# Kernel optimization log

Measured on AMD Instinct MI355X. Metric: run time of the kernel, lower is better.

## Reference

```python
import jax, jax.numpy as jnp
import numpy as np

IGNORE_INDEX = -100


def setup_inputs() -> dict:
    key = jax.random.key(0)
    k1, k2, k3 = jax.random.split(key, 3)
    N, H, V = 4096, 1024, 32000
    x = jax.random.normal(k1, (N, H), dtype=jnp.float32)
    # lm_head weight, laid out [H, V] so logits = x @ weight (kernel's [D, V] layout)
    weight = jax.random.normal(k2, (H, V), dtype=jnp.float32) * (1.0 / np.sqrt(H))
    target = jax.random.randint(k3, (N,), 0, V)
    # exercise the ignore_index masking path
    target = target.at[:64].set(IGNORE_INDEX)
    return {"x": x, "weight": weight, "target": target}


def reference(x, weight, target):
    # Fused linear + cross entropy, reduction='sum'.
    # logits: [N, V] (the tensor the fused kernel tiles to avoid materializing)
    logits = jnp.dot(x, weight)
    lse = jax.nn.logsumexp(logits, axis=-1)                  # [N]
    valid = target != IGNORE_INDEX                            # [N]
    safe_labels = jnp.where(valid, target, 0)
    target_logits = jnp.take_along_axis(logits, safe_labels[:, None], axis=-1)[:, 0]
    vmask = valid.astype(logits.dtype)
    losses = (lse - target_logits) * vmask                    # [N], 0 where ignored
    lse_masked = lse * vmask
    # reduction == 'sum'
    return losses.sum(), lse_masked.sum()
```

## Files before the change

### kernel.cpp

```cpp
#include <hip/hip_runtime.h>
#include <hip/hip_bf16.h>

typedef float f32x4 __attribute__((ext_vector_type(4)));
typedef int i32x4v __attribute__((ext_vector_type(4)));
typedef int i32x8v __attribute__((ext_vector_type(8)));

#define IGNORE_INDEX (-100)
#define N_ROWS 4096
#define H_DIM  1024
#define V_DIM  32000

#define BM 128
#define BN 256
#define BK 128
#define NKT (H_DIM / BK)
#define CT_NUM (V_DIM / BN)
#define RT_NUM (N_ROWS / BM)
#define SCALE1 0x7f7f7f7f

#define XB8 (N_ROWS * H_DIM / (256 * 16))
__global__ __launch_bounds__(256) void k_prep(const float* __restrict__ x,
                                              const float* __restrict__ w,
                                              unsigned char* __restrict__ x8,
                                              unsigned char* __restrict__ wT8) {
  __shared__ float tile[128][65];
  const int t = threadIdx.x;
  if (blockIdx.x < XB8) {
    size_t i = ((size_t)blockIdx.x * 256 + t) * 16;
    const float4* xp = (const float4*)(x + i);
    float4 f0 = xp[0], f1 = xp[1], f2 = xp[2], f3 = xp[3];
    int4 o;
    int r;
    r = __builtin_amdgcn_cvt_pk_fp8_f32(f0.x, f0.y, 0, false);
    r = __builtin_amdgcn_cvt_pk_fp8_f32(f0.z, f0.w, r, true);
    o.x = r;
    r = __builtin_amdgcn_cvt_pk_fp8_f32(f1.x, f1.y, 0, false);
    r = __builtin_amdgcn_cvt_pk_fp8_f32(f1.z, f1.w, r, true);
    o.y = r;
    r = __builtin_amdgcn_cvt_pk_fp8_f32(f2.x, f2.y, 0, false);
    r = __builtin_amdgcn_cvt_pk_fp8_f32(f2.z, f2.w, r, true);
    o.z = r;
    r = __builtin_amdgcn_cvt_pk_fp8_f32(f3.x, f3.y, 0, false);
    r = __builtin_amdgcn_cvt_pk_fp8_f32(f3.z, f3.w, r, true);
    o.w = r;
    *(int4*)(x8 + i) = o;
    return;
  }
  const int b = blockIdx.x - XB8;
  const int v0 = (b % (V_DIM / 64)) * 64;
  const int k0 = (b / (V_DIM / 64)) * 128;
  {
    const int vq = t & 15;
    const int kr = t >> 4;
#pragma unroll
    for (int p = 0; p < 128; p += 16) {
      float4 v = *(const float4*)(w + (size_t)(k0 + kr + p) * V_DIM + v0 + vq * 4);
      tile[kr + p][vq * 4 + 0] = v.x;
      tile[kr + p][vq * 4 + 1] = v.y;
      tile[kr + p][vq * 4 + 2] = v.z;
      tile[kr + p][vq * 4 + 3] = v.w;
    }
  }
  __syncthreads();
  {
    const int vr = t >> 2;
    const int kq2 = t & 3;
#pragma unroll
    for (int h = 0; h < 2; ++h) {
      const int d4 = kq2 + h * 4;
      int4 o;
      int r;
#pragma unroll
      for (int d = 0; d < 4; ++d) {
        r = __builtin_amdgcn_cvt_pk_fp8_f32(tile[d4 * 16 + d * 4 + 0][vr],
                                            tile[d4 * 16 + d * 4 + 1][vr], 0, false);
        r = __builtin_amdgcn_cvt_pk_fp8_f32(tile[d4 * 16 + d * 4 + 2][vr],
                                            tile[d4 * 16 + d * 4 + 3][vr], r, true);
        ((int*)&o)[d] = r;
      }
      *(int4*)(wT8 + (size_t)(v0 + vr) * H_DIM + k0 + d4 * 16) = o;
    }
  }
}

__global__ __launch_bounds__(256) void k_gemm_lse(const unsigned char* __restrict__ A,
                                                  const unsigned char* __restrict__ Bt,
                                                  float* __restrict__ m_part,
                                                  float* __restrict__ s_part) {
  extern __shared__ __align__(16) unsigned char sMemRaw[];
#define SMA(buf) (sMemRaw + (buf) * 49152)
#define SMB(buf) (sMemRaw + (buf) * 49152 + 16384)
  float* maxbuf = (float*)sMemRaw;
  float* sumbuf = (float*)(sMemRaw + 2048);

  const int tid = threadIdx.x;
  const int wg = ((int)blockIdx.x & 7) * ((RT_NUM * CT_NUM) / 8) + ((int)blockIdx.x >> 3);
  const int rt = wg & (RT_NUM - 1);
  const int ct = wg >> 5;
  const int m0 = rt * BM;
  const int n0 = ct * BN;

  const int w = tid >> 6;
  const int l = tid & 63;
  const int wm = w >> 1;
  const int wn = w & 1;
  const int quad = l >> 4, lc = l & 15;

  f32x4 acc[4][8];
#pragma unroll
  for (int i = 0; i < 4; ++i)
#pragma unroll
    for (int j = 0; j < 8; ++j)
      acc[i][j] = (f32x4){0.f, 0.f, 0.f, 0.f};

  const int srow = tid >> 3;
  const int scol = ((tid & 7) ^ (srow & 7)) * 16;
  const unsigned char* ga = A + (size_t)(m0 + srow) * H_DIM + scol;
  const unsigned char* gb = Bt + (size_t)(n0 + srow) * H_DIM + scol;
  const int dOff = tid * 16;

  const int aoff = wm * 8192 + lc * 128;
  const int boff = wn * 16384 + lc * 128;
  const int sw0 = ((quad * 2) ^ (lc & 7)) * 16;
  const int sw1 = ((quad * 2 + 1) ^ (lc & 7)) * 16;

#define GLDS(gp, lp)                                                     \
  __builtin_amdgcn_global_load_lds(                                      \
      (const __attribute__((address_space(1))) void*)(gp),               \
      (__attribute__((address_space(3))) void*)(lp), 16, 0, 0)

#define STAGE12(buf, koff)                                               \
  do {                                                                   \
    _Pragma("unroll")                                                    \
    for (int i_ = 0; i_ < 4; ++i_)                                       \
      GLDS(ga + (size_t)i_ * 32 * H_DIM + (koff),                        \
           SMA(buf) + dOff + i_ * 4096);                                 \
    _Pragma("unroll")                                                    \
    for (int i_ = 0; i_ < 8; ++i_)                                       \
      GLDS(gb + (size_t)i_ * 32 * H_DIM + (koff),                        \
           SMB(buf) + dOff + i_ * 4096);                                 \
  } while (0)

#define LDA8(dst, buf, i)                                                \
  do {                                                                   \
    const unsigned char* p_ = SMA(buf) + (i) * 2048 + aoff;              \
    i32x4v lo_ = *(const i32x4v*)(p_ + sw0);                             \
    i32x4v hi_ = *(const i32x4v*)(p_ + sw1);                             \
    dst = __builtin_shufflevector(lo_, hi_, 0, 1, 2, 3, 4, 5, 6, 7);     \
  } while (0)

#define LDB8(dst, buf, j)                                                \
  do {                                                                   \
    const unsigned char* p_ = SMB(buf) + (j) * 2048 + boff;              \
    i32x4v lo_ = *(const i32x4v*)(p_ + sw0);                             \
    i32x4v hi_ = *(const i32x4v*)(p_ + sw1);                             \
    dst = __builtin_shufflevector(lo_, hi_, 0, 1, 2, 3, 4, 5, 6, 7);     \
  } while (0)

  STAGE12(0, 0);
  __syncthreads();

#pragma unroll
  for (int kt = 0; kt < NKT; ++kt) {
    const int cur = kt & 1;
    if (kt < NKT - 1) STAGE12(cur ^ 1, (kt + 1) * BK);

    i32x8v af[4];
    LDA8(af[0], cur, 0); LDA8(af[1], cur, 1);
    LDA8(af[2], cur, 2); LDA8(af[3], cur, 3);
#pragma unroll
    for (int j = 0; j < 8; ++j) {
      i32x8v bfj;
      LDB8(bfj, cur, j);
#pragma unroll
      for (int i = 0; i < 4; ++i)
        acc[i][j] = __builtin_amdgcn_mfma_scale_f32_16x16x128_f8f6f4(
            af[i], bfj, acc[i][j], 0, 0, 0, SCALE1, 0, SCALE1);
    }
    __syncthreads();
  }
#undef STAGE12
#undef GLDS
#undef LDA8
#undef LDB8

  float rmax[4][4];
#pragma unroll
  for (int i = 0; i < 4; ++i)
#pragma unroll
    for (int r = 0; r < 4; ++r) {
      float mx = acc[i][0][r];
#pragma unroll
      for (int j = 1; j < 8; ++j) mx = fmaxf(mx, acc[i][j][r]);
#pragma unroll
      for (int off = 1; off < 16; off <<= 1)
        mx = fmaxf(mx, __shfl_xor(mx, off, 64));
      rmax[i][r] = mx;
    }
  if (lc == 0) {
#pragma unroll
    for (int i = 0; i < 4; ++i)
#pragma unroll
      for (int r = 0; r < 4; ++r)
        maxbuf[(wm * 64 + i * 16 + quad * 4 + r) * 2 + wn] = rmax[i][r];
  }
  __syncthreads();
  float rowmax[4][4];
#pragma unroll
  for (int i = 0; i < 4; ++i)
#pragma unroll
    for (int r = 0; r < 4; ++r) {
      int row = wm * 64 + i * 16 + quad * 4 + r;
      rowmax[i][r] = fmaxf(maxbuf[row * 2], maxbuf[row * 2 + 1]);
    }
#pragma unroll
  for (int i = 0; i < 4; ++i)
#pragma unroll
    for (int r = 0; r < 4; ++r) {
      float s = 0.f;
#pragma unroll
      for (int j = 0; j < 8; ++j) s += __expf(acc[i][j][r] - rowmax[i][r]);
#pragma unroll
      for (int off = 1; off < 16; off <<= 1)
        s += __shfl_xor(s, off, 64);
      if (lc == 0) sumbuf[(wm * 64 + i * 16 + quad * 4 + r) * 2 + wn] = s;
    }
  __syncthreads();
  if (wn == 0 && lc == 0) {
#pragma unroll
    for (int i = 0; i < 4; ++i)
#pragma unroll
      for (int r = 0; r < 4; ++r) {
        int row = wm * 64 + i * 16 + quad * 4 + r;
        size_t idx = (size_t)(m0 + row) * CT_NUM + ct;
        m_part[idx] = rowmax[i][r];
        s_part[idx] = sumbuf[row * 2] + sumbuf[row * 2 + 1];
      }
  }
#undef SMA
#undef SMB
}

__global__ __launch_bounds__(256) void k_combine(const float* __restrict__ x,
                                                 const unsigned char* __restrict__ wT8,
                                                 const int* __restrict__ target,
                                                 const float* __restrict__ m_part,
                                                 const float* __restrict__ s_part,
                                                 float* __restrict__ blk_part) {
  __shared__ float red[8];
  const int wv = threadIdx.x >> 6;
  const int row = blockIdx.x * 4 + wv;
  const int l = threadIdx.x & 63;
  float m = -INFINITY, s = 0.f;
  for (int ctb = l; ctb < CT_NUM; ctb += 64) {
    float mj = m_part[(size_t)row * CT_NUM + ctb];
    float sj = s_part[(size_t)row * CT_NUM + ctb];
    float M = fmaxf(m, mj);
    s = s * __expf(m - M) + sj * __expf(mj - M);
    m = M;
  }
#pragma unroll
  for (int off = 1; off < 64; off <<= 1) {
    float mo = __shfl_xor(m, off, 64);
    float so = __shfl_xor(s, off, 64);
    float M = fmaxf(m, mo);
    s = s * __expf(m - M) + so * __expf(mo - M);
    m = M;
  }
  float lse = m + logf(s);
  int tgt = target[row];
  bool valid = (tgt != IGNORE_INDEX);
  int st = valid ? tgt : 0;
  const float* xr = x + (size_t)row * H_DIM + l * 16;
  int4 wv4 = *(const int4*)(wT8 + (size_t)st * H_DIM + l * 16);
  float t = 0.f;
#define ACC_DW(dw, base)                                              \
  t += xr[base + 0] * __builtin_amdgcn_cvt_f32_fp8(dw, 0);            \
  t += xr[base + 1] * __builtin_amdgcn_cvt_f32_fp8(dw, 1);            \
  t += xr[base + 2] * __builtin_amdgcn_cvt_f32_fp8(dw, 2);            \
  t += xr[base + 3] * __builtin_amdgcn_cvt_f32_fp8(dw, 3);
  ACC_DW(wv4.x, 0)
  ACC_DW(wv4.y, 4)
  ACC_DW(wv4.z, 8)
  ACC_DW(wv4.w, 12)
#undef ACC_DW
#pragma unroll
  for (int off = 1; off < 64; off <<= 1)
    t += __shfl_xor(t, off, 64);
  if (l == 0) {
    red[wv * 2]     = valid ? (lse - t) : 0.f;
    red[wv * 2 + 1] = valid ? lse : 0.f;
  }
  __syncthreads();
  if (threadIdx.x == 0) {
    blk_part[blockIdx.x * 2]     = red[0] + red[2] + red[4] + red[6];
    blk_part[blockIdx.x * 2 + 1] = red[1] + red[3] + red[5] + red[7];
  }
}

__global__ __launch_bounds__(256) void k_final(const float* __restrict__ bp,
                                               float* __restrict__ out) {
  __shared__ float ra[4], rb[4];
  float a = 0.f, b = 0.f;
  for (int i = threadIdx.x; i < N_ROWS / 4; i += 256) {
    a += bp[i * 2];
    b += bp[i * 2 + 1];
  }
#pragma unroll
  for (int off = 1; off < 64; off <<= 1) {
    a += __shfl_xor(a, off, 64);
    b += __shfl_xor(b, off, 64);
  }
  if ((threadIdx.x & 63) == 0) { ra[threadIdx.x >> 6] = a; rb[threadIdx.x >> 6] = b; }
  __syncthreads();
  if (threadIdx.x == 0) {
    out[0] = ra[0] + ra[1] + ra[2] + ra[3];
    out[1] = rb[0] + rb[1] + rb[2] + rb[3];
  }
}

extern "C" void kernel_launch(void* const* d_in, const int* in_sizes, int n_in,
                              void* d_out, int out_size, void* d_ws, size_t ws_size,
                              hipStream_t stream) {
  const float* x = (const float*)d_in[0];
  const float* w = (const float*)d_in[1];
  const int* target = (const int*)d_in[2];
  float* out = (float*)d_out;

  static bool attr_set = false;
  if (!attr_set) {
    hipFuncSetAttribute(reinterpret_cast<const void*>(&k_gemm_lse),
                        hipFuncAttributeMaxDynamicSharedMemorySize, 98304);
    attr_set = true;
  }

  char* ws = (char*)d_ws;
  unsigned char* x8 = (unsigned char*)ws;
  unsigned char* wT8 = (unsigned char*)(ws + 4194304);
  float* m_part = (float*)(ws + 4194304 + 32768000);
  float* s_part = (float*)(ws + 4194304 + 32768000 + 2048000);
  float* blk_part = (float*)(ws + 4194304 + 32768000 + 2048000 + 2048000);

  k_prep<<<dim3(XB8 + (V_DIM / 64) * (H_DIM / 128)), 256, 0, stream>>>(x, w, x8, wT8);
  k_gemm_lse<<<dim3(RT_NUM * CT_NUM), 256, 98304, stream>>>(x8, wT8, m_part, s_part);
  k_combine<<<dim3(N_ROWS / 4), 256, 0, stream>>>(x, wT8, target, m_part, s_part, blk_part);
  k_final<<<dim3(1), 256, 0, stream>>>(blk_part, out);
}
```

Measured before the change: 449.3 us.

## Load A fragments directly from global into registers, shrink LDS staging

The A operand tiles are no longer staged through shared memory. Each wave now loads its MFMA A fragments directly from global memory into a double-buffered register array, and only B goes through global_load_lds. This cuts LDS usage from 96KB to 64KB per block, which may allow more resident blocks, and removes the LDS reads for A. The cost is more registers and uncoalesced 16-byte global loads for A, with each wave (wn=0 and wn=1) fetching the same rows redundantly.

```diff
diff --git a/kernel.cpp b/kernel.cpp
--- a/kernel.cpp
+++ b/kernel.cpp
@@ -88,8 +88,7 @@
                                                   float* __restrict__ m_part,
                                                   float* __restrict__ s_part) {
   extern __shared__ __align__(16) unsigned char sMemRaw[];
-#define SMA(buf) (sMemRaw + (buf) * 49152)
-#define SMB(buf) (sMemRaw + (buf) * 49152 + 16384)
+#define SMB(buf) (sMemRaw + (buf) * 32768)
   float* maxbuf = (float*)sMemRaw;
   float* sumbuf = (float*)(sMemRaw + 2048);
 
@@ -115,37 +114,33 @@
 
   const int srow = tid >> 3;
   const int scol = ((tid & 7) ^ (srow & 7)) * 16;
-  const unsigned char* ga = A + (size_t)(m0 + srow) * H_DIM + scol;
   const unsigned char* gb = Bt + (size_t)(n0 + srow) * H_DIM + scol;
   const int dOff = tid * 16;
 
-  const int aoff = wm * 8192 + lc * 128;
   const int boff = wn * 16384 + lc * 128;
   const int sw0 = ((quad * 2) ^ (lc & 7)) * 16;
   const int sw1 = ((quad * 2 + 1) ^ (lc & 7)) * 16;
+
+  const unsigned char* pa = A + (size_t)(m0 + wm * 64 + lc) * H_DIM + quad * 32;
 
 #define GLDS(gp, lp)                                                     \
   __builtin_amdgcn_global_load_lds(                                      \
       (const __attribute__((address_space(1))) void*)(gp),               \
       (__attribute__((address_space(3))) void*)(lp), 16, 0, 0)
 
-#define STAGE12(buf, koff)                                               \
+#define STAGE8(buf, koff)                                                \
   do {                                                                   \
-    _Pragma("unroll")                                                    \
-    for (int i_ = 0; i_ < 4; ++i_)                                       \
-      GLDS(ga + (size_t)i_ * 32 * H_DIM + (koff),                        \
-           SMA(buf) + dOff + i_ * 4096);                                 \
     _Pragma("unroll")                                                    \
     for (int i_ = 0; i_ < 8; ++i_)                                       \
       GLDS(gb + (size_t)i_ * 32 * H_DIM + (koff),                        \
            SMB(buf) + dOff + i_ * 4096);                                 \
   } while (0)
 
-#define LDA8(dst, buf, i)                                                \
+#define LDAG(dst, i, koff)                                               \
   do {                                                                   \
-    const unsigned char* p_ = SMA(buf) + (i) * 2048 + aoff;              \
-    i32x4v lo_ = *(const i32x4v*)(p_ + sw0);                             \
-    i32x4v hi_ = *(const i32x4v*)(p_ + sw1);                             \
+    const unsigned char* p_ = pa + (size_t)(i) * 16 * H_DIM + (koff);    \
+    i32x4v lo_ = *(const i32x4v*)(p_);                                   \
+    i32x4v hi_ = *(const i32x4v*)(p_ + 16);                              \
     dst = __builtin_shufflevector(lo_, hi_, 0, 1, 2, 3, 4, 5, 6, 7);     \
   } while (0)
 
@@ -157,17 +152,23 @@
     dst = __builtin_shufflevector(lo_, hi_, 0, 1, 2, 3, 4, 5, 6, 7);     \
   } while (0)
 
-  STAGE12(0, 0);
+  i32x8v af[2][4];
+
+  STAGE8(0, 0);
+  LDAG(af[0][0], 0, 0); LDAG(af[0][1], 1, 0);
+  LDAG(af[0][2], 2, 0); LDAG(af[0][3], 3, 0);
   __syncthreads();
 
 #pragma unroll
   for (int kt = 0; kt < NKT; ++kt) {
     const int cur = kt & 1;
-    if (kt < NKT - 1) STAGE12(cur ^ 1, (kt + 1) * BK);
-
-    i32x8v af[4];
-    LDA8(af[0], cur, 0); LDA8(af[1], cur, 1);
-    LDA8(af[2], cur, 2); LDA8(af[3], cur, 3);
+    const int nk = cur ^ 1;
+    if (kt < NKT - 1) {
+      const int koff = (kt + 1) * BK;
+      STAGE8(nk, koff);
+      LDAG(af[nk][0], 0, koff); LDAG(af[nk][1], 1, koff);
+      LDAG(af[nk][2], 2, koff); LDAG(af[nk][3], 3, koff);
+    }
 #pragma unroll
     for (int j = 0; j < 8; ++j) {
       i32x8v bfj;
@@ -175,13 +176,13 @@
 #pragma unroll
       for (int i = 0; i < 4; ++i)
         acc[i][j] = __builtin_amdgcn_mfma_scale_f32_16x16x128_f8f6f4(
-            af[i], bfj, acc[i][j], 0, 0, 0, SCALE1, 0, SCALE1);
+            af[cur][i], bfj, acc[i][j], 0, 0, 0, SCALE1, 0, SCALE1);
     }
     __syncthreads();
   }
-#undef STAGE12
+#undef STAGE8
 #undef GLDS
-#undef LDA8
+#undef LDAG
 #undef LDB8
 
   float rmax[4][4];
@@ -237,7 +238,6 @@
         s_part[idx] = sumbuf[row * 2] + sumbuf[row * 2 + 1];
       }
   }
-#undef SMA
 #undef SMB
 }
 
@@ -330,7 +330,7 @@
   static bool attr_set = false;
   if (!attr_set) {
     hipFuncSetAttribute(reinterpret_cast<const void*>(&k_gemm_lse),
-                        hipFuncAttributeMaxDynamicSharedMemorySize, 98304);
+                        hipFuncAttributeMaxDynamicSharedMemorySize, 65536);
     attr_set = true;
   }
 
@@ -342,7 +342,7 @@
   float* blk_part = (float*)(ws + 4194304 + 32768000 + 2048000 + 2048000);
 
   k_prep<<<dim3(XB8 + (V_DIM / 64) * (H_DIM / 128)), 256, 0, stream>>>(x, w, x8, wT8);
-  k_gemm_lse<<<dim3(RT_NUM * CT_NUM), 256, 98304, stream>>>(x8, wT8, m_part, s_part);
+  k_gemm_lse<<<dim3(RT_NUM * CT_NUM), 256, 65536, stream>>>(x8, wT8, m_part, s_part);
   k_combine<<<dim3(N_ROWS / 4), 256, 0, stream>>>(x, wT8, target, m_part, s_part, blk_part);
   k_final<<<dim3(1), 256, 0, stream>>>(blk_part, out);
 }
```

New measurement: 508.0 us. +13.1%, slower.
